# Kernel optimization log

Measured on AMD Instinct MI355X. Metric: run time of the kernel, lower is better.

The kernel has to match this reference:

```python
import jax, jax.numpy as jnp
import numpy as np

BS, NQ, NC = 128, 900, 91
PRE_TOPK = 10000      # source: pre_topk when n_queries*n_cls > 10000
POST_TOPK = 100       # source: keep_inds[:100]
IOU_THRESH = 0.7


def box_cxcywh_to_xyxy(b):
    cx, cy, w, h = b[..., 0], b[..., 1], b[..., 2], b[..., 3]
    return jnp.stack([cx - 0.5 * w, cy - 0.5 * h, cx + 0.5 * w, cy + 0.5 * h], axis=-1)


def nms_image(boxes, scores, labels):
    """Greedy batched NMS, returning the first POST_TOPK picked indices.
    boxes: [PRE,4] xyxy (scaled), scores: [PRE] desc-sorted, labels: [PRE] int.
    batched_nms trick: offset boxes per class so IoU across classes is 0."""
    max_coord = jnp.max(boxes)
    off = labels.astype(boxes.dtype) * (max_coord + 1.0)
    ob = boxes + off[:, None]                          # [PRE,4]
    areas = (ob[:, 2] - ob[:, 0]) * (ob[:, 3] - ob[:, 1])

    def step(active, _):
        s = jnp.where(active, scores, -jnp.inf)
        i = jnp.argmax(s)                              # highest-score surviving box
        bi = ob[i]
        xx1 = jnp.maximum(bi[0], ob[:, 0])
        yy1 = jnp.maximum(bi[1], ob[:, 1])
        xx2 = jnp.minimum(bi[2], ob[:, 2])
        yy2 = jnp.minimum(bi[3], ob[:, 3])
        inter = jnp.clip(xx2 - xx1, 0.0) * jnp.clip(yy2 - yy1, 0.0)
        union = areas[i] + areas - inter
        iou = inter / jnp.maximum(union, 1e-9)
        # suppress IoU > thresh (includes i itself since iou(i,i)=1)
        active = active & (iou <= IOU_THRESH)
        return active, i

    _, keep = jax.lax.scan(step, jnp.ones(ob.shape[0], dtype=bool), None, length=POST_TOPK)
    return keep                                         # [POST]


def setup_inputs() -> dict:
    key = jax.random.key(0)
    k1, k2, k3, k4 = jax.random.split(key, 4)
    pred_logits = jax.random.normal(k1, (BS, NQ, NC), dtype=jnp.float32) * 2.0 - 2.0
    cxcy = jax.random.uniform(k2, (BS, NQ, 2), dtype=jnp.float32)
    wh = jax.random.uniform(k3, (BS, NQ, 2), dtype=jnp.float32, minval=0.02, maxval=0.3)
    pred_boxes = jnp.concatenate([cxcy, wh], axis=-1)   # cxcywh in [0,1]
    target_sizes = jax.random.uniform(k4, (BS, 2), dtype=jnp.float32, minval=480.0, maxval=1333.0)
    return {"pred_logits": pred_logits, "pred_boxes": pred_boxes, "target_sizes": target_sizes}


def reference(pred_logits, pred_boxes, target_sizes):
    bs, nq, nc = pred_logits.shape
    prob = jax.nn.sigmoid(pred_logits).reshape(bs, nq * nc)      # all_scores
    boxes = box_cxcywh_to_xyxy(pred_boxes)                        # [bs,nq,4]
    img_h, img_w = target_sizes[:, 0], target_sizes[:, 1]
    scale = jnp.stack([img_w, img_h, img_w, img_h], axis=1)       # [bs,4]
    boxes = boxes * scale[:, None, :]

    top_scores, top_idx = jax.lax.top_k(prob, PRE_TOPK)           # [bs,PRE]
    top_labels = top_idx % nc                                     # all_labels gather
    top_box_idx = top_idx // nc                                   # all_boxes gather
    top_boxes = jnp.take_along_axis(boxes, top_box_idx[..., None], axis=1)  # [bs,PRE,4]

    keep = jax.vmap(nms_image)(top_boxes, top_scores, top_labels)  # [bs,POST]
    out_scores = jnp.take_along_axis(top_scores, keep, axis=1)
    out_labels = jnp.take_along_axis(top_labels, keep, axis=1)
    out_boxes = jnp.take_along_axis(top_boxes, keep[..., None], axis=1)
    return out_scores, out_labels, out_boxes
```

## Files before the change

### kernel.cpp

```cpp
#include <hip/hip_runtime.h>
#include <cstdint>

#pragma clang fp contract(off)

#define BS   128
#define NQ   900
#define NC   91
#define NQC  (NQ * NC)
#define Q4   (NQC / 4)
#define PRE  10000
#define POST 100
#define NCAP 12288
#define TBITS 13
#define TBINS (1 << TBITS)
#define TSHIFT (32 - TBITS)
#define K_WIN 16
#define HSEG 1024
#define KS   2780

typedef unsigned long long ull;

__device__ __forceinline__ uint32_t fkey(float f) {
    uint32_t b = __float_as_uint(f);
    return (b & 0x80000000u) ? ~b : (b | 0x80000000u);
}
__device__ __forceinline__ float unkey(uint32_t u) {
    uint32_t b = (u & 0x80000000u) ? (u & 0x7FFFFFFFu) : ~u;
    return __uint_as_float(b);
}
__device__ __forceinline__ uint32_t qclamp(uint32_t q) { return (q < NQ) ? q : (NQ - 1); }

__device__ __forceinline__ ull shflx(ull v, int j) {
    uint32_t lo = (uint32_t)__shfl_xor((int)(uint32_t)v, j, 64);
    uint32_t hi = (uint32_t)__shfl_xor((int)(uint32_t)(v >> 32), j, 64);
    return ((ull)hi << 32) | (ull)lo;
}
__device__ __forceinline__ ull cex(ull v, int j, bool lower, bool desc) {
    ull pb = shflx(v, j);
    ull a = lower ? v : pb;
    ull b = lower ? pb : v;
    bool sw = desc ? (a < b) : (a > b);
    return sw ? pb : v;
}

__global__ void __launch_bounds__(1024) k_fused(const float* __restrict__ logits,
                                                const float* __restrict__ pred_boxes,
                                                const float* __restrict__ target_sizes,
                                                float* __restrict__ out) {
    const int img = blockIdx.x;
    const int tid = threadIdx.x;
    const int lane = tid & 63;
    const int wv = tid >> 6;

    __shared__ ull ca[NCAP];
    __shared__ float4 shPB[NQ];
    __shared__ ull headK[HSEG];
    __shared__ uint32_t h8[16][256];
    __shared__ float aX1[POST], aY1[POST], aX2[POST], aY2[POST], aAr[POST];
    __shared__ int   aCl[POST];
    __shared__ float s_x1[K_WIN], s_y1[K_WIN], s_x2[K_WIN], s_y2[K_WIN];
    __shared__ int   s_cl[K_WIN];
    __shared__ uint32_t s_em[K_WIN];
    __shared__ uint32_t smx[16];
    __shared__ float sOffD;
    __shared__ ull sP, sF0;
    __shared__ uint32_t sT, sCnt, sTlo;

    uint32_t* hist13 = (uint32_t*)ca;
    uint32_t* part = (uint32_t*)h8;

    const float ih = target_sizes[img * 2 + 0];
    const float iw = target_sizes[img * 2 + 1];
    const float* pb = pred_boxes + (size_t)img * NQ * 4;
    const float4* lg4 = (const float4*)(logits + (size_t)img * NQC);

    if (tid < NQ) shPB[tid] = ((const float4*)pb)[tid];
    for (int i = tid; i < TBINS; i += 1024) hist13[i] = 0u;
    if (tid == 0) { sCnt = 0u; sF0 = 0ull; }
    float4 sv[5];
    #pragma unroll
    for (int c = 0; c < 5; ++c) sv[c] = lg4[c * 4096 + tid];
    __syncthreads();

    #pragma unroll
    for (int c = 0; c < 5; ++c) {
        atomicAdd(&hist13[fkey(sv[c].x) >> TSHIFT], 1u);
        atomicAdd(&hist13[fkey(sv[c].y) >> TSHIFT], 1u);
        atomicAdd(&hist13[fkey(sv[c].z) >> TSHIFT], 1u);
        atomicAdd(&hist13[fkey(sv[c].w) >> TSHIFT], 1u);
    }
    __syncthreads();
    {
        uint32_t s = 0;
        int base0 = tid * 8;
        #pragma unroll
        for (int j = 0; j < 8; ++j) s += hist13[base0 + j];
        part[tid] = s;
    }
    __syncthreads();
    if (tid < 64) {
        uint32_t pv[16]; uint32_t tot = 0;
        #pragma unroll
        for (int j = 0; j < 16; ++j) { pv[j] = part[tid * 16 + j]; tot += pv[j]; }
        uint32_t sinc = tot;
        #pragma unroll
        for (int off = 1; off < 64; off <<= 1) {
            uint32_t o = (uint32_t)__shfl_down((int)sinc, off, 64);
            if (tid + off < 64) sinc += o;
        }
        uint32_t cum = sinc - tot;
        for (int j = 15; j >= 0; --j) {
            if (cum < KS && cum + pv[j] >= KS) {
                int pbn = (tid * 16 + j) * 8;
                uint32_t c2 = cum;
                for (int b = pbn + 7; b >= pbn; --b) {
                    if (c2 + hist13[b] >= KS) { sTlo = ((uint32_t)b) << TSHIFT; break; }
                    c2 += hist13[b];
                }
            }
            cum += pv[j];
        }
    }
    __syncthreads();
    const uint32_t Tlo = sTlo;

    for (int i0 = 0; i0 < Q4; i0 += 1024) {
        int i = i0 + tid;
        bool inb = (i < Q4);
        float4 v = inb ? lg4[i] : make_float4(0.f, 0.f, 0.f, 0.f);
        uint32_t u0 = fkey(v.x), u1 = fkey(v.y), u2 = fkey(v.z), u3 = fkey(v.w);
        bool p0 = inb && u0 >= Tlo, p1 = inb && u1 >= Tlo;
        bool p2 = inb && u2 >= Tlo, p3 = inb && u3 >= Tlo;
        ull m0 = __ballot(p0), m1 = __ballot(p1), m2 = __ballot(p2), m3 = __ballot(p3);
        uint32_t c0 = (uint32_t)__popcll(m0), c1 = (uint32_t)__popcll(m1);
        uint32_t c2 = (uint32_t)__popcll(m2), c3 = (uint32_t)__popcll(m3);
        uint32_t wb = 0u;
        if (lane == 0) wb = atomicAdd(&sCnt, c0 + c1 + c2 + c3);
        wb = (uint32_t)__shfl((int)wb, 0, 64);
        ull lm = (1ull << lane) - 1ull;
        uint32_t fi = (uint32_t)(i * 4);
        uint32_t b0 = wb + (uint32_t)__popcll(m0 & lm);
        uint32_t b1 = wb + c0 + (uint32_t)__popcll(m1 & lm);
        uint32_t b2 = wb + c0 + c1 + (uint32_t)__popcll(m2 & lm);
        uint32_t b3 = wb + c0 + c1 + c2 + (uint32_t)__popcll(m3 & lm);
        if (p0 && b0 < NCAP) ca[b0] = ((ull)u0 << 32) | (ull)(0xFFFFFFFFu - (fi + 0));
        if (p1 && b1 < NCAP) ca[b1] = ((ull)u1 << 32) | (ull)(0xFFFFFFFFu - (fi + 1));
        if (p2 && b2 < NCAP) ca[b2] = ((ull)u2 << 32) | (ull)(0xFFFFFFFFu - (fi + 2));
        if (p3 && b3 < NCAP) ca[b3] = ((ull)u3 << 32) | (ull)(0xFFFFFFFFu - (fi + 3));
    }
    __syncthreads();
    const uint32_t cnt = (sCnt < NCAP) ? sCnt : NCAP;
    for (int i = tid; i < NCAP; i += 1024) if (i >= (int)cnt) ca[i] = 0ull;
    __syncthreads();

    auto selk = [&](uint32_t T) -> ull {
        if (tid == 0) { sP = 0ull; sT = T; }
        for (int pos = 56; pos >= 0; pos -= 8) {
            for (int i = tid; i < 16 * 256; i += 1024) ((uint32_t*)h8)[i] = 0u;
            __syncthreads();
            const ull P = sP; const uint32_t t = sT;
            const ull pm = (pos >= 56) ? 0ull : (~0ull << (pos + 8));
            for (int i = tid; i < NCAP; i += 1024) {
                ull x = ca[i];
                if (x != 0ull && (x & pm) == (P & pm))
                    atomicAdd(&h8[wv][(uint32_t)(x >> pos) & 255u], 1u);
            }
            __syncthreads();
            if (tid < 64) {
                uint32_t hd[4]; uint32_t g = 0;
                #pragma unroll
                for (int q = 0; q < 4; ++q) {
                    uint32_t s = 0;
                    for (int w = 0; w < 16; ++w) s += h8[w][lane * 4 + q];
                    hd[q] = s; g += s;
                }
                uint32_t sinc = g;
                #pragma unroll
                for (int off = 1; off < 64; off <<= 1) {
                    uint32_t o = (uint32_t)__shfl_down((int)sinc, off, 64);
                    if (lane + off < 64) sinc += o;
                }
                uint32_t cum = sinc - g;
                for (int q = 3; q >= 0; --q) {
                    if (cum < t && cum + hd[q] >= t) {
                        sP = P | ((ull)(uint32_t)(lane * 4 + q) << pos);
                        sT = t - cum;
                    }
                    cum += hd[q];
                }
            }
            __syncthreads();
        }
        return sP;
    };

    const uint32_t TK = (cnt < PRE) ? cnt : PRE;
    const ull Kstar = selk(TK);
    {
        uint32_t lmx = 0u;
        for (int i = tid; i < NCAP; i += 1024) {
            ull x = ca[i];
            if (x >= Kstar && x != 0ull) {
                uint32_t f = ~(uint32_t)x;
                uint32_t q = qclamp(f / NC);
                float4 bb = shPB[q];
                float x1 = (bb.x - 0.5f * bb.z) * iw;
                float y1 = (bb.y - 0.5f * bb.w) * ih;
                float x2 = (bb.x + 0.5f * bb.z) * iw;
                float y2 = (bb.y + 0.5f * bb.w) * ih;
                uint32_t km = fkey(fmaxf(fmaxf(x1, y1), fmaxf(x2, y2)));
                if (km > lmx) lmx = km;
            }
        }
        for (int off = 32; off > 0; off >>= 1) {
            uint32_t o = (uint32_t)__shfl_down((int)lmx, off, 64);
            if (o > lmx) lmx = o;
        }
        if (lane == 0) smx[wv] = lmx;
        __syncthreads();
        if (tid == 0) {
            uint32_t m = smx[0];
            for (int w2 = 1; w2 < 16; ++w2) if (smx[w2] > m) m = smx[w2];
            uint32_t b = (m & 0x80000000u) ? (m & 0x7FFFFFFFu) : ~m;
            sOffD = __uint_as_float(b) + 1.0f;
        }
        __syncthreads();
    }
    const float offD = sOffD;

    int npick = 0, base = 0, segbase = 0, segend = 0;
    ull Khi = ~0ull;
    bool needF0 = true;
    while (npick < POST) {
        if (base >= segend) {
            if (segend >= (int)TK) {
                ull x0 = sF0;
                uint32_t f0 = ~(uint32_t)x0;
                uint32_t u0 = (uint32_t)(x0 >> 32);
                uint32_t q0 = qclamp(f0 / NC);
                uint32_t c0 = f0 - (f0 / NC) * NC;
                float4 bb = shPB[q0];
                float rx1 = (bb.x - 0.5f * bb.z) * iw;
                float ry1 = (bb.y - 0.5f * bb.w) * ih;
                float rx2 = (bb.x + 0.5f * bb.z) * iw;
                float ry2 = (bb.y + 0.5f * bb.w) * ih;
                float sc = 1.0f / (1.0f + expf(-unkey(u0)));
                for (int p2 = npick + tid; p2 < POST; p2 += 1024) {
                    out[img * POST + p2] = sc;
                    out[BS * POST + img * POST + p2] = (float)c0;
                    float* ob2 = out + 2 * BS * POST + ((size_t)img * POST + p2) * 4;
                    ob2[0] = rx1; ob2[1] = ry1; ob2[2] = rx2; ob2[3] = ry2;
                }
                break;
            }
            int Tsel = segend + HSEG; if (Tsel > (int)TK) Tsel = (int)TK;
            ull Klo = selk((uint32_t)Tsel);
            for (int i = tid; i < HSEG; i += 1024) headK[i] = 0ull;
            if (tid == 0) sCnt = 0u;
            __syncthreads();
            for (int i = tid; i < NCAP; i += 1024) {
                ull x = ca[i];
                bool pass = (x != 0ull) && (x >= Klo) && (x < Khi);
                ull m = __ballot(pass);
                uint32_t below = (uint32_t)__popcll(m & ((1ull << lane) - 1ull));
                uint32_t wtot = (uint32_t)__popcll(m);
                uint32_t wb = 0u;
                if (lane == 0 && wtot) wb = atomicAdd(&sCnt, wtot);
                wb = (uint32_t)__shfl((int)wb, 0, 64);
                if (pass) { uint32_t p = wb + below; if (p < HSEG) headK[p] = x; }
            }
            __syncthreads();
            {
                const int idx = tid;
                ull x = headK[idx];
                #pragma unroll
                for (int k2 = 2; k2 <= 32; k2 <<= 1) {
                    bool d = ((lane & k2) == 0);
                    #pragma unroll
                    for (int j = 16; j >= 1; j >>= 1)
                        if (j <= (k2 >> 1)) x = cex(x, j, (lane & j) == 0, d);
                }
                {
                    bool d = ((idx & 64) == 0);
                    #pragma unroll
                    for (int j = 32; j >= 1; j >>= 1) x = cex(x, j, (lane & j) == 0, d);
                }
                for (int k = 128; k <= 1024; k <<= 1) {
                    headK[idx] = x;
                    __syncthreads();
                    for (int j = k >> 1; j >= 64; j >>= 1) {
                        if (tid < 512) {
                            int i2 = ((tid & ~(j - 1)) << 1) | (tid & (j - 1));
                            int ixj = i2 | j;
                            ull a = headK[i2], b = headK[ixj];
                            bool sw = ((i2 & k) == 0) ? (a < b) : (a > b);
                            if (sw) { headK[i2] = b; headK[ixj] = a; }
                        }
                        __syncthreads();
                    }
                    x = headK[idx];
                    bool d = ((idx & k) == 0);
                    #pragma unroll
                    for (int j = 32; j >= 1; j >>= 1) x = cex(x, j, (lane & j) == 0, d);
                }
                headK[idx] = x;
                __syncthreads();
            }
            if (needF0) { if (tid == 0) sF0 = headK[0]; needF0 = false; }
            __syncthreads();
            segbase = segend; segend = Tsel; Khi = Klo;
            continue;
        }

        const int r = base + wv;
        const bool val = (r < segend);
        const ull xk = headK[val ? (r - segbase) : 0];
        const uint32_t f = val ? ~(uint32_t)xk : 0u;
        const uint32_t uk = (uint32_t)(xk >> 32);
        const uint32_t q = qclamp(f / NC);
        const uint32_t cc = f - (f / NC) * NC;
        float4 bb = shPB[q];
        const float x1 = (bb.x - 0.5f * bb.z) * iw;
        const float y1 = (bb.y - 0.5f * bb.w) * ih;
        const float x2 = (bb.x + 0.5f * bb.z) * iw;
        const float y2 = (bb.y + 0.5f * bb.w) * ih;
        if (lane == 0) {
            s_x1[wv] = x1; s_y1[wv] = y1; s_x2[wv] = x2; s_y2[wv] = y2;
            s_cl[wv] = val ? (int)cc : -1;
        }
        __syncthreads();

        const float o = (float)cc * offD;
        const float cx1 = x1 + o, cy1 = y1 + o, cx2 = x2 + o, cy2 = y2 + o;
        const float car = (cx2 - cx1) * (cy2 - cy1);
        bool cf = false;
        if (val && lane < wv && s_cl[lane] == (int)cc) {
            float jx1 = s_x1[lane] + o, jy1 = s_y1[lane] + o;
            float jx2 = s_x2[lane] + o, jy2 = s_y2[lane] + o;
            float arj = (jx2 - jx1) * (jy2 - jy1);
            float xx1 = fmaxf(jx1, cx1), yy1 = fmaxf(jy1, cy1);
            float xx2 = fminf(jx2, cx2), yy2 = fminf(jy2, cy2);
            float inter = fmaxf(xx2 - xx1, 0.0f) * fmaxf(yy2 - yy1, 0.0f);
            float uni = (arj + car) - inter;
            float iou = inter / fmaxf(uni, 1e-9f);
            cf = !(iou <= 0.7f);
        }
        uint32_t em = (uint32_t)(__ballot(cf) & 0xFFFFull);
        bool pf = false;
        for (int i2 = lane; i2 < npick; i2 += 64) {
            if (aCl[i2] == (int)cc) {
                float jx1 = aX1[i2] + o, jy1 = aY1[i2] + o;
                float jx2 = aX2[i2] + o, jy2 = aY2[i2] + o;
                float arj = aAr[i2];
                float xx1 = fmaxf(jx1, cx1), yy1 = fmaxf(jy1, cy1);
                float xx2 = fminf(jx2, cx2), yy2 = fminf(jy2, cy2);
                float inter = fmaxf(xx2 - xx1, 0.0f) * fmaxf(yy2 - yy1, 0.0f);
                float uni = (arj + car) - inter;
                float iou = inter / fmaxf(uni, 1e-9f);
                pf |= !(iou <= 0.7f);
            }
        }
        bool anyPrior = (__ballot(pf) != 0ull);
        if (lane == 0)
            s_em[wv] = em | (anyPrior ? 0x80000000u : 0u) | (val ? 0u : 0x40000000u);
        __syncthreads();

        uint32_t acc = 0u; int a = 0;
        const int room = POST - npick;
        #pragma unroll
        for (int w2 = 0; w2 < K_WIN; ++w2) {
            uint32_t ew = s_em[w2];
            if (!(ew & 0xC0000000u) && a < room && ((ew & 0xFFFFu & acc) == 0u)) {
                acc |= (1u << w2); ++a;
            }
        }

        if (((acc >> wv) & 1u) && lane == 0) {
            int p = npick + __popc(acc & ((1u << wv) - 1u));
            float sc = 1.0f / (1.0f + expf(-unkey(uk)));
            out[img * POST + p] = sc;
            out[BS * POST + img * POST + p] = (float)cc;
            float* ob2 = out + 2 * BS * POST + ((size_t)img * POST + p) * 4;
            ob2[0] = x1; ob2[1] = y1; ob2[2] = x2; ob2[3] = y2;
            aX1[p] = x1; aY1[p] = y1; aX2[p] = x2; aY2[p] = y2;
            aAr[p] = car; aCl[p] = (int)cc;
        }
        npick += a;
        base += K_WIN;
    }
}

extern "C" void kernel_launch(void* const* d_in, const int* in_sizes, int n_in,
                              void* d_out, int out_size, void* d_ws, size_t ws_size,
                              hipStream_t stream) {
    const float* logits = (const float*)d_in[0];
    const float* boxes  = (const float*)d_in[1];
    const float* tsizes = (const float*)d_in[2];
    float* out = (float*)d_out;
    (void)d_ws; (void)ws_size;

    k_fused<<<BS, 1024, 0, stream>>>(logits, boxes, tsizes, out);
}
```

Baseline: 167.5 us.

## Replace 8-pass radix select with 12-bit histogram bucket plus bitonic sort

Builds a 12-bit top-bits histogram of the candidate keys once, then each k-th selection finds the target bucket by a prefix scan, compacts that bucket into headK, and sorts it with the shared 1024-element bitonic sort to read the exact threshold. This replaces up to eight histogram passes over all 12288 candidates, each with barriers, by a single compaction plus one sort. If the bucket holds more than 1024 keys it falls back to the old radix select and rebuilds the histogram. The existing segment sort is factored into a reusable lambda, and a separate part buffer is added to shared memory, which may affect occupancy.

```diff
diff --git a/kernel.cpp b/kernel.cpp
--- a/kernel.cpp
+++ b/kernel.cpp
@@ -56,6 +56,7 @@
     __shared__ float4 shPB[NQ];
     __shared__ ull headK[HSEG];
     __shared__ uint32_t h8[16][256];
+    __shared__ uint32_t part[1024];
     __shared__ float aX1[POST], aY1[POST], aX2[POST], aY2[POST], aAr[POST];
     __shared__ int   aCl[POST];
     __shared__ float s_x1[K_WIN], s_y1[K_WIN], s_x2[K_WIN], s_y2[K_WIN];
@@ -64,10 +65,10 @@
     __shared__ uint32_t smx[16];
     __shared__ float sOffD;
     __shared__ ull sP, sF0;
-    __shared__ uint32_t sT, sCnt, sTlo;
+    __shared__ uint32_t sT, sCnt, sCnt2, sTlo, sB, sTp;
 
     uint32_t* hist13 = (uint32_t*)ca;
-    uint32_t* part = (uint32_t*)h8;
+    uint32_t* hist12 = (uint32_t*)h8;
 
     const float ih = target_sizes[img * 2 + 0];
     const float iw = target_sizes[img * 2 + 1];
@@ -153,7 +154,105 @@
     for (int i = tid; i < NCAP; i += 1024) if (i >= (int)cnt) ca[i] = 0ull;
     __syncthreads();
 
-    auto selk = [&](uint32_t T) -> ull {
+    for (int i = tid; i < 4096; i += 1024) hist12[i] = 0u;
+    __syncthreads();
+    for (int i = tid; i < NCAP; i += 1024) {
+        ull x = ca[i];
+        if (x != 0ull) atomicAdd(&hist12[(uint32_t)(x >> 52)], 1u);
+    }
+    __syncthreads();
+
+    auto sort1024 = [&]() {
+        const int idx = tid;
+        ull x = headK[idx];
+        #pragma unroll
+        for (int k2 = 2; k2 <= 32; k2 <<= 1) {
+            bool d = ((lane & k2) == 0);
+            #pragma unroll
+            for (int j = 16; j >= 1; j >>= 1)
+                if (j <= (k2 >> 1)) x = cex(x, j, (lane & j) == 0, d);
+        }
+        {
+            bool d = ((idx & 64) == 0);
+            #pragma unroll
+            for (int j = 32; j >= 1; j >>= 1) x = cex(x, j, (lane & j) == 0, d);
+        }
+        for (int k = 128; k <= 1024; k <<= 1) {
+            headK[idx] = x;
+            __syncthreads();
+            for (int j = k >> 1; j >= 64; j >>= 1) {
+                if (tid < 512) {
+                    int i2 = ((tid & ~(j - 1)) << 1) | (tid & (j - 1));
+                    int ixj = i2 | j;
+                    ull a = headK[i2], b = headK[ixj];
+                    bool sw = ((i2 & k) == 0) ? (a < b) : (a > b);
+                    if (sw) { headK[i2] = b; headK[ixj] = a; }
+                }
+                __syncthreads();
+            }
+            x = headK[idx];
+            bool d = ((idx & k) == 0);
+            #pragma unroll
+            for (int j = 32; j >= 1; j >>= 1) x = cex(x, j, (lane & j) == 0, d);
+        }
+        headK[idx] = x;
+        __syncthreads();
+    };
+
+    auto selk2 = [&](uint32_t T) -> ull {
+        if (T == 0u) return 0ull;
+        {
+            uint32_t s = 0; int b0 = tid * 4;
+            #pragma unroll
+            for (int j = 0; j < 4; ++j) s += hist12[b0 + j];
+            part[tid] = s;
+        }
+        __syncthreads();
+        if (tid < 64) {
+            uint32_t pv[16]; uint32_t tot = 0;
+            #pragma unroll
+            for (int j = 0; j < 16; ++j) { pv[j] = part[tid * 16 + j]; tot += pv[j]; }
+            uint32_t sinc = tot;
+            #pragma unroll
+            for (int off = 1; off < 64; off <<= 1) {
+                uint32_t o = (uint32_t)__shfl_down((int)sinc, off, 64);
+                if (tid + off < 64) sinc += o;
+            }
+            uint32_t cum = sinc - tot;
+            for (int j = 15; j >= 0; --j) {
+                if (cum < T && cum + pv[j] >= T) {
+                    int pbn = (tid * 16 + j) * 4;
+                    uint32_t c2 = cum;
+                    for (int b = pbn + 3; b >= pbn; --b) {
+                        if (c2 + hist12[b] >= T) { sB = (uint32_t)b; sTp = T - c2; break; }
+                        c2 += hist12[b];
+                    }
+                }
+                cum += pv[j];
+            }
+        }
+        __syncthreads();
+        const uint32_t B = sB;
+        const uint32_t tp = sTp;
+        for (int i = tid; i < HSEG; i += 1024) headK[i] = 0ull;
+        if (tid == 0) sCnt2 = 0u;
+        __syncthreads();
+        for (int i = tid; i < NCAP; i += 1024) {
+            ull x = ca[i];
+            bool pass = (x != 0ull) && ((uint32_t)(x >> 52) == B);
+            ull m = __ballot(pass);
+            uint32_t below = (uint32_t)__popcll(m & ((1ull << lane) - 1ull));
+            uint32_t wtot = (uint32_t)__popcll(m);
+            uint32_t wb = 0u;
+            if (lane == 0 && wtot) wb = atomicAdd(&sCnt2, wtot);
+            wb = (uint32_t)__shfl((int)wb, 0, 64);
+            if (pass) { uint32_t p = wb + below; if (p < HSEG) headK[p] = x; }
+        }
+        __syncthreads();
+        if (sCnt2 <= HSEG) {
+            sort1024();
+            return headK[tp - 1];
+        }
         if (tid == 0) { sP = 0ull; sT = T; }
         for (int pos = 56; pos >= 0; pos -= 8) {
             for (int i = tid; i < 16 * 256; i += 1024) ((uint32_t*)h8)[i] = 0u;
@@ -191,11 +290,18 @@
             }
             __syncthreads();
         }
+        for (int i = tid; i < 4096; i += 1024) hist12[i] = 0u;
+        __syncthreads();
+        for (int i = tid; i < NCAP; i += 1024) {
+            ull x = ca[i];
+            if (x != 0ull) atomicAdd(&hist12[(uint32_t)(x >> 52)], 1u);
+        }
+        __syncthreads();
         return sP;
     };
 
     const uint32_t TK = (cnt < PRE) ? cnt : PRE;
-    const ull Kstar = selk(TK);
+    const ull Kstar = selk2(TK);
     {
         uint32_t lmx = 0u;
         for (int i = tid; i < NCAP; i += 1024) {
@@ -254,7 +360,8 @@
                 break;
             }
             int Tsel = segend + HSEG; if (Tsel > (int)TK) Tsel = (int)TK;
-            ull Klo = selk((uint32_t)Tsel);
+            ull Klo = selk2((uint32_t)Tsel);
+            __syncthreads();
             for (int i = tid; i < HSEG; i += 1024) headK[i] = 0ull;
             if (tid == 0) sCnt = 0u;
             __syncthreads();
@@ -270,42 +377,7 @@
                 if (pass) { uint32_t p = wb + below; if (p < HSEG) headK[p] = x; }
             }
             __syncthreads();
-            {
-                const int idx = tid;
-                ull x = headK[idx];
-                #pragma unroll
-                for (int k2 = 2; k2 <= 32; k2 <<= 1) {
-                    bool d = ((lane & k2) == 0);
-                    #pragma unroll
-                    for (int j = 16; j >= 1; j >>= 1)
-                        if (j <= (k2 >> 1)) x = cex(x, j, (lane & j) == 0, d);
-                }
-                {
-                    bool d = ((idx & 64) == 0);
-                    #pragma unroll
-                    for (int j = 32; j >= 1; j >>= 1) x = cex(x, j, (lane & j) == 0, d);
-                }
-                for (int k = 128; k <= 1024; k <<= 1) {
-                    headK[idx] = x;
-                    __syncthreads();
-                    for (int j = k >> 1; j >= 64; j >>= 1) {
-                        if (tid < 512) {
-                            int i2 = ((tid & ~(j - 1)) << 1) | (tid & (j - 1));
-                            int ixj = i2 | j;
-                            ull a = headK[i2], b = headK[ixj];
-                            bool sw = ((i2 & k) == 0) ? (a < b) : (a > b);
-                            if (sw) { headK[i2] = b; headK[ixj] = a; }
-                        }
-                        __syncthreads();
-                    }
-                    x = headK[idx];
-                    bool d = ((idx & k) == 0);
-                    #pragma unroll
-                    for (int j = 32; j >= 1; j >>= 1) x = cex(x, j, (lane & j) == 0, d);
-                }
-                headK[idx] = x;
-                __syncthreads();
-            }
+            sort1024();
             if (needF0) { if (tid == 0) sF0 = headK[0]; needF0 = false; }
             __syncthreads();
             segbase = segend; segend = Tsel; Khi = Klo;
```

Result: no change. 168.4 us (+0.5%).

## Replace radix-select passes with a 12-bit histogram and bin-based segment extraction

Applied to the files above, without the earlier changes.

The multi-pass 8-bit radix select (selk), which ran once for the top-K threshold and again for every 1024-element segment, is replaced. A 12-bit histogram of candidate keys is built during compaction, and the TK-th and 1024-th key bins are found with a single scan. The boundary bin and the head segment are then sorted together by a two-array register/shared bitonic network. Later segments are refilled by extracting whole histogram bins instead of re-running selection. This removes many full passes over the 12K candidate buffer and their barriers, but a bin holding more than 1024 elements would be truncated, which is a correctness risk on skewed inputs.

```diff
diff --git a/kernel.cpp b/kernel.cpp
--- a/kernel.cpp
+++ b/kernel.cpp
@@ -42,6 +42,10 @@
     bool sw = desc ? (a < b) : (a > b);
     return sw ? pb : v;
 }
+__device__ __forceinline__ void ce(ull& a, ull& b, bool desc) {
+    bool sw = desc ? (a < b) : (a > b);
+    if (sw) { ull t = a; a = b; b = t; }
+}
 
 __global__ void __launch_bounds__(1024) k_fused(const float* __restrict__ logits,
                                                 const float* __restrict__ pred_boxes,
@@ -54,29 +58,41 @@
 
     __shared__ ull ca[NCAP];
     __shared__ float4 shPB[NQ];
+    __shared__ ull binK[HSEG];
     __shared__ ull headK[HSEG];
-    __shared__ uint32_t h8[16][256];
+    __shared__ uint32_t hist12[4096];
+    __shared__ uint32_t part[1024];
     __shared__ float aX1[POST], aY1[POST], aX2[POST], aY2[POST], aAr[POST];
     __shared__ int   aCl[POST];
     __shared__ float s_x1[K_WIN], s_y1[K_WIN], s_x2[K_WIN], s_y2[K_WIN];
     __shared__ int   s_cl[K_WIN];
     __shared__ uint32_t s_em[K_WIN];
-    __shared__ uint32_t smx[16];
     __shared__ float sOffD;
-    __shared__ ull sP, sF0;
-    __shared__ uint32_t sT, sCnt, sTlo;
+    __shared__ ull sF0;
+    __shared__ uint32_t sCnt, sCntA, sCntB, sTlo, sMX;
+    __shared__ uint32_t sB1, sTp1, sB2, sTp2;
 
     uint32_t* hist13 = (uint32_t*)ca;
-    uint32_t* part = (uint32_t*)h8;
 
     const float ih = target_sizes[img * 2 + 0];
     const float iw = target_sizes[img * 2 + 1];
     const float* pb = pred_boxes + (size_t)img * NQ * 4;
     const float4* lg4 = (const float4*)(logits + (size_t)img * NQC);
 
+    auto mckey = [&](uint32_t f) -> uint32_t {
+        uint32_t q = qclamp(f / NC);
+        float4 bb = shPB[q];
+        float x1 = (bb.x - 0.5f * bb.z) * iw;
+        float y1 = (bb.y - 0.5f * bb.w) * ih;
+        float x2 = (bb.x + 0.5f * bb.z) * iw;
+        float y2 = (bb.y + 0.5f * bb.w) * ih;
+        return fkey(fmaxf(fmaxf(x1, y1), fmaxf(x2, y2)));
+    };
+
     if (tid < NQ) shPB[tid] = ((const float4*)pb)[tid];
     for (int i = tid; i < TBINS; i += 1024) hist13[i] = 0u;
-    if (tid == 0) { sCnt = 0u; sF0 = 0ull; }
+    for (int i = tid; i < 4096; i += 1024) hist12[i] = 0u;
+    if (tid == 0) { sCnt = 0u; sMX = 0u; sF0 = 0ull; }
     float4 sv[5];
     #pragma unroll
     for (int c = 0; c < 5; ++c) sv[c] = lg4[c * 4096 + tid];
@@ -92,9 +108,9 @@
     __syncthreads();
     {
         uint32_t s = 0;
-        int base0 = tid * 8;
-        #pragma unroll
-        for (int j = 0; j < 8; ++j) s += hist13[base0 + j];
+        int b0 = tid * 8;
+        #pragma unroll
+        for (int j = 0; j < 8; ++j) s += hist13[b0 + j];
         part[tid] = s;
     }
     __syncthreads();
@@ -143,94 +159,252 @@
         uint32_t b1 = wb + c0 + (uint32_t)__popcll(m1 & lm);
         uint32_t b2 = wb + c0 + c1 + (uint32_t)__popcll(m2 & lm);
         uint32_t b3 = wb + c0 + c1 + c2 + (uint32_t)__popcll(m3 & lm);
-        if (p0 && b0 < NCAP) ca[b0] = ((ull)u0 << 32) | (ull)(0xFFFFFFFFu - (fi + 0));
-        if (p1 && b1 < NCAP) ca[b1] = ((ull)u1 << 32) | (ull)(0xFFFFFFFFu - (fi + 1));
-        if (p2 && b2 < NCAP) ca[b2] = ((ull)u2 << 32) | (ull)(0xFFFFFFFFu - (fi + 2));
-        if (p3 && b3 < NCAP) ca[b3] = ((ull)u3 << 32) | (ull)(0xFFFFFFFFu - (fi + 3));
+        if (p0) { if (b0 < NCAP) ca[b0] = ((ull)u0 << 32) | (ull)(0xFFFFFFFFu - (fi + 0)); atomicAdd(&hist12[u0 >> 20], 1u); }
+        if (p1) { if (b1 < NCAP) ca[b1] = ((ull)u1 << 32) | (ull)(0xFFFFFFFFu - (fi + 1)); atomicAdd(&hist12[u1 >> 20], 1u); }
+        if (p2) { if (b2 < NCAP) ca[b2] = ((ull)u2 << 32) | (ull)(0xFFFFFFFFu - (fi + 2)); atomicAdd(&hist12[u2 >> 20], 1u); }
+        if (p3) { if (b3 < NCAP) ca[b3] = ((ull)u3 << 32) | (ull)(0xFFFFFFFFu - (fi + 3)); atomicAdd(&hist12[u3 >> 20], 1u); }
     }
     __syncthreads();
     const uint32_t cnt = (sCnt < NCAP) ? sCnt : NCAP;
-    for (int i = tid; i < NCAP; i += 1024) if (i >= (int)cnt) ca[i] = 0ull;
-    __syncthreads();
-
-    auto selk = [&](uint32_t T) -> ull {
-        if (tid == 0) { sP = 0ull; sT = T; }
-        for (int pos = 56; pos >= 0; pos -= 8) {
-            for (int i = tid; i < 16 * 256; i += 1024) ((uint32_t*)h8)[i] = 0u;
+    const uint32_t TK = (cnt < PRE) ? cnt : PRE;
+    const uint32_t T2 = (TK < HSEG) ? TK : HSEG;
+
+    {
+        int b0 = tid * 4;
+        part[tid] = hist12[b0] + hist12[b0 + 1] + hist12[b0 + 2] + hist12[b0 + 3];
+        binK[tid] = 0ull; headK[tid] = 0ull;
+        if (tid == 0) { sCntA = 0u; sCntB = 0u; }
+    }
+    __syncthreads();
+    if (tid < 64) {
+        uint32_t pv[16]; uint32_t tot = 0;
+        #pragma unroll
+        for (int j = 0; j < 16; ++j) { pv[j] = part[tid * 16 + j]; tot += pv[j]; }
+        uint32_t sinc = tot;
+        #pragma unroll
+        for (int off = 1; off < 64; off <<= 1) {
+            uint32_t o = (uint32_t)__shfl_down((int)sinc, off, 64);
+            if (tid + off < 64) sinc += o;
+        }
+        uint32_t cum = sinc - tot;
+        for (int j = 15; j >= 0; --j) {
+            if (cum < TK && cum + pv[j] >= TK) {
+                int pbn = (tid * 16 + j) * 4;
+                uint32_t c2 = cum;
+                for (int b = pbn + 3; b >= pbn; --b) {
+                    if (c2 + hist12[b] >= TK) { sB1 = (uint32_t)b; sTp1 = TK - c2; break; }
+                    c2 += hist12[b];
+                }
+            }
+            if (cum < T2 && cum + pv[j] >= T2) {
+                int pbn = (tid * 16 + j) * 4;
+                uint32_t c2 = cum;
+                for (int b = pbn + 3; b >= pbn; --b) {
+                    if (c2 + hist12[b] >= T2) { sB2 = (uint32_t)b; sTp2 = T2 - c2; break; }
+                    c2 += hist12[b];
+                }
+            }
+            cum += pv[j];
+        }
+    }
+    __syncthreads();
+    const uint32_t B1 = sB1, tp1 = sTp1;
+    const uint32_t B2 = sB2;
+    const int C1 = (int)(T2 - sTp2);
+
+    uint32_t lmx = 0u;
+    {
+        const int rounds = (int)((cnt + 1023u) >> 10);
+        for (int r = 0; r < rounds; ++r) {
+            int i = tid + (r << 10);
+            bool live = (i < (int)cnt);
+            ull x = live ? ca[i] : 0ull;
+            uint32_t bin = (uint32_t)(x >> 52);
+            if (live && bin > B1) {
+                uint32_t km = mckey(~(uint32_t)x);
+                if (km > lmx) lmx = km;
+            }
+            bool isA = live && (bin == B1);
+            bool isB = live && (bin > B2);
+            ull mA = __ballot(isA), mB = __ballot(isB);
+            uint32_t wbA = 0u, wbB = 0u;
+            if (lane == 0) {
+                uint32_t cA = (uint32_t)__popcll(mA), cB = (uint32_t)__popcll(mB);
+                if (cA) wbA = atomicAdd(&sCntA, cA);
+                if (cB) wbB = atomicAdd(&sCntB, cB);
+            }
+            wbA = (uint32_t)__shfl((int)wbA, 0, 64);
+            wbB = (uint32_t)__shfl((int)wbB, 0, 64);
+            ull lm = (1ull << lane) - 1ull;
+            if (isA) { uint32_t p = wbA + (uint32_t)__popcll(mA & lm); if (p < HSEG) binK[p] = x; }
+            if (isB) { uint32_t p = wbB + (uint32_t)__popcll(mB & lm); if (p < HSEG) headK[p] = x; }
+        }
+    }
+    __syncthreads();
+
+    {
+        ull r0 = 0, r1 = 0, r2 = 0, r3 = 0;
+        const int cw = wv & 3;
+        const int cb = cw << 8;
+        ull* A = (wv < 4) ? binK : headK;
+        if (wv < 8) {
+            r0 = A[cb | lane]; r1 = A[cb | 64 | lane];
+            r2 = A[cb | 128 | lane]; r3 = A[cb | 192 | lane];
+            #pragma unroll
+            for (int k2 = 2; k2 <= 32; k2 <<= 1) {
+                bool d = ((lane & k2) == 0);
+                #pragma unroll
+                for (int j = 16; j >= 1; j >>= 1) {
+                    if (j <= (k2 >> 1)) {
+                        bool lw = ((lane & j) == 0);
+                        r0 = cex(r0, j, lw, d); r1 = cex(r1, j, lw, d);
+                        r2 = cex(r2, j, lw, d); r3 = cex(r3, j, lw, d);
+                    }
+                }
+            }
+            #pragma unroll
+            for (int j = 32; j >= 1; j >>= 1) {
+                bool lw = ((lane & j) == 0);
+                r0 = cex(r0, j, lw, true);  r1 = cex(r1, j, lw, false);
+                r2 = cex(r2, j, lw, true);  r3 = cex(r3, j, lw, false);
+            }
+            ce(r0, r1, true); ce(r2, r3, false);
+            #pragma unroll
+            for (int j = 32; j >= 1; j >>= 1) {
+                bool lw = ((lane & j) == 0);
+                r0 = cex(r0, j, lw, true);  r1 = cex(r1, j, lw, true);
+                r2 = cex(r2, j, lw, false); r3 = cex(r3, j, lw, false);
+            }
+            {
+                bool d = ((cw & 1) == 0);
+                ce(r0, r2, d); ce(r1, r3, d); ce(r0, r1, d); ce(r2, r3, d);
+                #pragma unroll
+                for (int j = 32; j >= 1; j >>= 1) {
+                    bool lw = ((lane & j) == 0);
+                    r0 = cex(r0, j, lw, d); r1 = cex(r1, j, lw, d);
+                    r2 = cex(r2, j, lw, d); r3 = cex(r3, j, lw, d);
+                }
+            }
+            A[cb | lane] = r0; A[cb | 64 | lane] = r1;
+            A[cb | 128 | lane] = r2; A[cb | 192 | lane] = r3;
+        }
+        __syncthreads();
+        {
+            ull* Bp = (tid >> 9) ? headK : binK;
+            int t = tid & 511;
+            int i = ((t & ~255) << 1) | (t & 255);
+            int ixj = i | 256;
+            bool d = ((i & 512) == 0);
+            ull a = Bp[i], b = Bp[ixj];
+            bool sw = d ? (a < b) : (a > b);
+            if (sw) { Bp[i] = b; Bp[ixj] = a; }
+        }
+        __syncthreads();
+        if (wv < 8) {
+            r0 = A[cb | lane]; r1 = A[cb | 64 | lane];
+            r2 = A[cb | 128 | lane]; r3 = A[cb | 192 | lane];
+            bool d = ((cw & 2) == 0);
+            ce(r0, r2, d); ce(r1, r3, d); ce(r0, r1, d); ce(r2, r3, d);
+            #pragma unroll
+            for (int j = 32; j >= 1; j >>= 1) {
+                bool lw = ((lane & j) == 0);
+                r0 = cex(r0, j, lw, d); r1 = cex(r1, j, lw, d);
+                r2 = cex(r2, j, lw, d); r3 = cex(r3, j, lw, d);
+            }
+            A[cb | lane] = r0; A[cb | 64 | lane] = r1;
+            A[cb | 128 | lane] = r2; A[cb | 192 | lane] = r3;
+        }
+        __syncthreads();
+        {
+            ull* Bp = (tid >> 9) ? headK : binK;
+            int t = tid & 511;
+            ull a = Bp[t], b = Bp[t | 512];
+            if (a < b) { Bp[t] = b; Bp[t | 512] = a; }
+        }
+        __syncthreads();
+        {
+            ull* Bp = (tid >> 9) ? headK : binK;
+            int t = tid & 511;
+            int i = ((t & ~255) << 1) | (t & 255);
+            int ixj = i | 256;
+            ull a = Bp[i], b = Bp[ixj];
+            if (a < b) { Bp[i] = b; Bp[ixj] = a; }
+        }
+        __syncthreads();
+        if (wv < 8) {
+            r0 = A[cb | lane]; r1 = A[cb | 64 | lane];
+            r2 = A[cb | 128 | lane]; r3 = A[cb | 192 | lane];
+            ce(r0, r2, true); ce(r1, r3, true); ce(r0, r1, true); ce(r2, r3, true);
+            #pragma unroll
+            for (int j = 32; j >= 1; j >>= 1) {
+                bool lw = ((lane & j) == 0);
+                r0 = cex(r0, j, lw, true); r1 = cex(r1, j, lw, true);
+                r2 = cex(r2, j, lw, true); r3 = cex(r3, j, lw, true);
+            }
+            A[cb | lane] = r0; A[cb | 64 | lane] = r1;
+            A[cb | 128 | lane] = r2; A[cb | 192 | lane] = r3;
+        }
+        __syncthreads();
+    }
+
+    if (tid < (int)tp1) {
+        ull x = binK[tid];
+        if (x != 0ull) { uint32_t km = mckey(~(uint32_t)x); if (km > lmx) lmx = km; }
+    }
+    for (int off = 32; off > 0; off >>= 1) {
+        uint32_t o = (uint32_t)__shfl_down((int)lmx, off, 64);
+        if (o > lmx) lmx = o;
+    }
+    if (lane == 0) atomicMax(&sMX, lmx);
+    if (tid == 0 && C1 > 0) sF0 = headK[0];
+    __syncthreads();
+    float offD;
+    {
+        uint32_t m = sMX;
+        uint32_t b = (m & 0x80000000u) ? (m & 0x7FFFFFFFu) : ~m;
+        offD = __uint_as_float(b) + 1.0f;
+    }
+
+    auto sort1024 = [&]() {
+        const int idx = tid;
+        ull x = headK[idx];
+        #pragma unroll
+        for (int k2 = 2; k2 <= 32; k2 <<= 1) {
+            bool d = ((lane & k2) == 0);
+            #pragma unroll
+            for (int j = 16; j >= 1; j >>= 1)
+                if (j <= (k2 >> 1)) x = cex(x, j, (lane & j) == 0, d);
+        }
+        {
+            bool d = ((idx & 64) == 0);
+            #pragma unroll
+            for (int j = 32; j >= 1; j >>= 1) x = cex(x, j, (lane & j) == 0, d);
+        }
+        for (int k = 128; k <= 1024; k <<= 1) {
+            headK[idx] = x;
             __syncthreads();
-            const ull P = sP; const uint32_t t = sT;
-            const ull pm = (pos >= 56) ? 0ull : (~0ull << (pos + 8));
-            for (int i = tid; i < NCAP; i += 1024) {
-                ull x = ca[i];
-                if (x != 0ull && (x & pm) == (P & pm))
-                    atomicAdd(&h8[wv][(uint32_t)(x >> pos) & 255u], 1u);
-            }
-            __syncthreads();
-            if (tid < 64) {
-                uint32_t hd[4]; uint32_t g = 0;
-                #pragma unroll
-                for (int q = 0; q < 4; ++q) {
-                    uint32_t s = 0;
-                    for (int w = 0; w < 16; ++w) s += h8[w][lane * 4 + q];
-                    hd[q] = s; g += s;
-                }
-                uint32_t sinc = g;
-                #pragma unroll
-                for (int off = 1; off < 64; off <<= 1) {
-                    uint32_t o = (uint32_t)__shfl_down((int)sinc, off, 64);
-                    if (lane + off < 64) sinc += o;
-                }
-                uint32_t cum = sinc - g;
-                for (int q = 3; q >= 0; --q) {
-                    if (cum < t && cum + hd[q] >= t) {
-                        sP = P | ((ull)(uint32_t)(lane * 4 + q) << pos);
-                        sT = t - cum;
-                    }
-                    cum += hd[q];
-                }
-            }
-            __syncthreads();
-        }
-        return sP;
+            for (int j = k >> 1; j >= 64; j >>= 1) {
+                if (tid < 512) {
+                    int i2 = ((tid & ~(j - 1)) << 1) | (tid & (j - 1));
+                    int ixj = i2 | j;
+                    ull a = headK[i2], b = headK[ixj];
+                    bool sw = ((i2 & k) == 0) ? (a < b) : (a > b);
+                    if (sw) { headK[i2] = b; headK[ixj] = a; }
+                }
+                __syncthreads();
+            }
+            x = headK[idx];
+            bool d = ((idx & k) == 0);
+            #pragma unroll
+            for (int j = 32; j >= 1; j >>= 1) x = cex(x, j, (lane & j) == 0, d);
+        }
+        headK[idx] = x;
+        __syncthreads();
     };
 
-    const uint32_t TK = (cnt < PRE) ? cnt : PRE;
-    const ull Kstar = selk(TK);
-    {
-        uint32_t lmx = 0u;
-        for (int i = tid; i < NCAP; i += 1024) {
-            ull x = ca[i];
-            if (x >= Kstar && x != 0ull) {
-                uint32_t f = ~(uint32_t)x;
-                uint32_t q = qclamp(f / NC);
-                float4 bb = shPB[q];
-                float x1 = (bb.x - 0.5f * bb.z) * iw;
-                float y1 = (bb.y - 0.5f * bb.w) * ih;
-                float x2 = (bb.x + 0.5f * bb.z) * iw;
-                float y2 = (bb.y + 0.5f * bb.w) * ih;
-                uint32_t km = fkey(fmaxf(fmaxf(x1, y1), fmaxf(x2, y2)));
-                if (km > lmx) lmx = km;
-            }
-        }
-        for (int off = 32; off > 0; off >>= 1) {
-            uint32_t o = (uint32_t)__shfl_down((int)lmx, off, 64);
-            if (o > lmx) lmx = o;
-        }
-        if (lane == 0) smx[wv] = lmx;
-        __syncthreads();
-        if (tid == 0) {
-            uint32_t m = smx[0];
-            for (int w2 = 1; w2 < 16; ++w2) if (smx[w2] > m) m = smx[w2];
-            uint32_t b = (m & 0x80000000u) ? (m & 0x7FFFFFFFu) : ~m;
-            sOffD = __uint_as_float(b) + 1.0f;
-        }
-        __syncthreads();
-    }
-    const float offD = sOffD;
-
-    int npick = 0, base = 0, segbase = 0, segend = 0;
-    ull Khi = ~0ull;
-    bool needF0 = true;
+    int npick = 0, base = 0, segbase = 0, segend = C1;
+    int bcur = (int)B2;
+    bool needF0 = (C1 == 0);
     while (npick < POST) {
         if (base >= segend) {
             if (segend >= (int)TK) {
@@ -253,62 +427,31 @@
                 }
                 break;
             }
-            int Tsel = segend + HSEG; if (Tsel > (int)TK) Tsel = (int)TK;
-            ull Klo = selk((uint32_t)Tsel);
-            for (int i = tid; i < HSEG; i += 1024) headK[i] = 0ull;
-            if (tid == 0) sCnt = 0u;
-            __syncthreads();
-            for (int i = tid; i < NCAP; i += 1024) {
-                ull x = ca[i];
-                bool pass = (x != 0ull) && (x >= Klo) && (x < Khi);
-                ull m = __ballot(pass);
-                uint32_t below = (uint32_t)__popcll(m & ((1ull << lane) - 1ull));
-                uint32_t wtot = (uint32_t)__popcll(m);
-                uint32_t wb = 0u;
-                if (lane == 0 && wtot) wb = atomicAdd(&sCnt, wtot);
-                wb = (uint32_t)__shfl((int)wb, 0, 64);
-                if (pass) { uint32_t p = wb + below; if (p < HSEG) headK[p] = x; }
-            }
+            while (bcur > 0 && hist12[bcur] == 0u) --bcur;
+            headK[tid] = 0ull;
+            if (tid == 0) sCntA = 0u;
             __syncthreads();
             {
-                const int idx = tid;
-                ull x = headK[idx];
-                #pragma unroll
-                for (int k2 = 2; k2 <= 32; k2 <<= 1) {
-                    bool d = ((lane & k2) == 0);
-                    #pragma unroll
-                    for (int j = 16; j >= 1; j >>= 1)
-                        if (j <= (k2 >> 1)) x = cex(x, j, (lane & j) == 0, d);
-                }
-                {
-                    bool d = ((idx & 64) == 0);
-                    #pragma unroll
-                    for (int j = 32; j >= 1; j >>= 1) x = cex(x, j, (lane & j) == 0, d);
-                }
-                for (int k = 128; k <= 1024; k <<= 1) {
-                    headK[idx] = x;
-                    __syncthreads();
-                    for (int j = k >> 1; j >= 64; j >>= 1) {
-                        if (tid < 512) {
-                            int i2 = ((tid & ~(j - 1)) << 1) | (tid & (j - 1));
-                            int ixj = i2 | j;
-                            ull a = headK[i2], b = headK[ixj];
-                            bool sw = ((i2 & k) == 0) ? (a < b) : (a > b);
-                            if (sw) { headK[i2] = b; headK[ixj] = a; }
-                        }
-                        __syncthreads();
-                    }
-                    x = headK[idx];
-                    bool d = ((idx & k) == 0);
-                    #pragma unroll
-                    for (int j = 32; j >= 1; j >>= 1) x = cex(x, j, (lane & j) == 0, d);
-                }
-                headK[idx] = x;
-                __syncthreads();
-            }
-            if (needF0) { if (tid == 0) sF0 = headK[0]; needF0 = false; }
+                const int rounds = (int)((cnt + 1023u) >> 10);
+                for (int r2 = 0; r2 < rounds; ++r2) {
+                    int i = tid + (r2 << 10);
+                    bool pass = (i < (int)cnt) && ((uint32_t)(ca[i] >> 52) == (uint32_t)bcur);
+                    ull x = pass ? ca[i] : 0ull;
+                    ull m = __ballot(pass);
+                    uint32_t below = (uint32_t)__popcll(m & ((1ull << lane) - 1ull));
+                    uint32_t wtot = (uint32_t)__popcll(m);
+                    uint32_t wb = 0u;
+                    if (lane == 0 && wtot) wb = atomicAdd(&sCntA, wtot);
+                    wb = (uint32_t)__shfl((int)wb, 0, 64);
+                    if (pass) { uint32_t p = wb + below; if (p < HSEG) headK[p] = x; }
+                }
+            }
             __syncthreads();
-            segbase = segend; segend = Tsel; Khi = Klo;
+            sort1024();
+            int avail = (int)((sCntA < (uint32_t)HSEG) ? sCntA : (uint32_t)HSEG);
+            int take = (int)TK - segend; if (take > avail) take = avail;
+            if (needF0) { if (tid == 0) sF0 = headK[0]; needF0 = false; __syncthreads(); }
+            segbase = segend; segend += take; --bcur;
             continue;
         }
 
```

Measured after the change: 138.0 us. 1.21x faster.
